# Performance work log

Measured on AMD Instinct MI355X. Metric: run time of the kernel, lower is better.

The kernel has to match this reference:

```python
import jax, jax.numpy as jnp
import numpy as np

L = 32768          # sequence length (keys/values)
E = 1024           # embed_dim (hardcoded in module via weight slices)
H, D = 8, 128      # num_heads, head_dim (hardcoded via reshape(-1, 8, 128))


def setup_inputs() -> dict:
    key = jax.random.key(0)
    k1, k2, k3, k4, k5 = jax.random.split(key, 5)
    scale = 1.0 / np.sqrt(E)
    return {
        "x": jax.random.normal(k1, (L, E), dtype=jnp.float32),
        "in_proj_weight": jax.random.normal(k2, (3 * E, E), dtype=jnp.float32) * scale,
        "in_proj_bias": jax.random.normal(k3, (3 * E,), dtype=jnp.float32) * 0.02,
        "out_proj_weight": jax.random.normal(k4, (E, E), dtype=jnp.float32) * scale,
        "out_proj_bias": jax.random.normal(k5, (E,), dtype=jnp.float32) * 0.02,
    }


def reference(x, in_proj_weight, in_proj_bias, out_proj_weight, out_proj_bias):
    # Single-query (decode-style) attention: q from first token only.
    q = x[:1] @ in_proj_weight[:E].T + in_proj_bias[:E]              # [1, E]
    k = x @ in_proj_weight[E:2 * E].T + in_proj_bias[E:2 * E]        # [L, E]
    v = x @ in_proj_weight[2 * E:].T + in_proj_bias[2 * E:]          # [L, E]

    q = q.reshape(-1, H, D).transpose(1, 0, 2)                       # [H, 1, D]
    k = k.reshape(-1, H, D).transpose(1, 2, 0)                       # [H, D, L]
    v = v.reshape(-1, H, D).transpose(1, 0, 2)                       # [H, L, D]

    dot = jnp.matmul(q, k) * (1.0 / np.sqrt(D))                      # [H, 1, L]
    attn = jax.nn.softmax(dot, axis=-1)
    out = jnp.matmul(attn, v)                                        # [H, 1, D]

    out = out.transpose(1, 0, 2).reshape(-1, E)                      # [1, E]
    out = out @ out_proj_weight.T + out_proj_bias                    # [1, E]
    return out
```

## Files before the change

kernel.cpp:

```cpp
#include <hip/hip_runtime.h>
#include <math.h>


#define L_SEQ   32768
#define E_DIM   1024
#define NHEAD   8
#define HDIM    128
#define TILE_R  8
#define WAVES_M 8

__global__ __launch_bounds__(256) void proj_q(
    const float* __restrict__ W, const float* __restrict__ bias,
    const float* __restrict__ x, float* __restrict__ q)
{
  const int t = threadIdx.x, wave = t >> 6, lane = t & 63;
  const int o = blockIdx.x * 4 + wave;
  const float4* Wr = (const float4*)(W + (size_t)o * E_DIM);
  const float4* xr = (const float4*)x;
  float a = 0.f;
#pragma unroll
  for (int k = 0; k < 4; ++k) {
    float4 wv = Wr[lane + 64 * k];
    float4 xv = xr[lane + 64 * k];
    a += wv.x * xv.x + wv.y * xv.y + wv.z * xv.z + wv.w * xv.w;
  }
#pragma unroll
  for (int m = 1; m < 64; m <<= 1) a += __shfl_xor(a, m, 64);
  if (lane == 0) q[o] = a + bias[o];
}

__global__ __launch_bounds__(128) void make_p(
    const float* __restrict__ W, const float* __restrict__ q,
    float* __restrict__ P_T)
{
  const int h = blockIdx.y;
  const int e = blockIdx.x * 128 + threadIdx.x;
  const float* qh = q + h * HDIM;
  const float* Wb = W + ((size_t)E_DIM + (size_t)h * HDIM) * E_DIM + e;
  float a0 = 0.f, a1 = 0.f, a2 = 0.f, a3 = 0.f;
#pragma unroll 4
  for (int d = 0; d < HDIM; d += 4) {
    a0 += qh[d + 0] * Wb[(size_t)(d + 0) * E_DIM];
    a1 += qh[d + 1] * Wb[(size_t)(d + 1) * E_DIM];
    a2 += qh[d + 2] * Wb[(size_t)(d + 2) * E_DIM];
    a3 += qh[d + 3] * Wb[(size_t)(d + 3) * E_DIM];
  }
  P_T[h * E_DIM + e] = ((a0 + a1) + (a2 + a3)) * 0.08838834764831845f;
}

__global__ __launch_bounds__(512, 2) void attn_fused5(
    const float* __restrict__ x,
    const float* __restrict__ P_T,
    float* __restrict__ partial_z,
    float* __restrict__ partial_sumw,
    int rows_per_blk)
{
  __shared__ __align__(16) float x_tile[2][TILE_R][E_DIM];
  __shared__ __align__(16) float w_tile[TILE_R][NHEAD];
  __shared__ __align__(16) float sw_stage[WAVES_M][4];

  const int t = threadIdx.x;
  const int wave = t >> 6;
  const int lane = t & 63;
  const size_t row0 = (size_t)blockIdx.x * rows_per_blk;
  const int ntiles = rows_per_blk / TILE_R;
  const int rg = wave >> 1;
  const int hg = wave & 1;

  const int r_l = lane & 1;
  const int h_l = (((lane >> 1) & 1) << 1) | ((lane >> 2) & 1);

  float4 p[4][4];
#pragma unroll
  for (int j = 0; j < 4; ++j) {
    const float4* pr = (const float4*)(P_T + (size_t)(4 * hg + j) * E_DIM);
#pragma unroll
    for (int k = 0; k < 4; ++k) p[j][k] = pr[lane + 64 * k];
  }

  float acc[16];
#pragma unroll
  for (int i = 0; i < 16; ++i) acc[i] = 0.f;
  float sumw_own = 0.f;

  {
    const float* g = x + (row0 + wave) * E_DIM;
#pragma unroll
    for (int k = 0; k < 4; ++k)
      __builtin_amdgcn_global_load_lds(
          (const __attribute__((address_space(1))) void*)(g + k * 256 + lane * 4),
          (__attribute__((address_space(3))) void*)(&x_tile[0][wave][k * 256]),
          16, 0, 0);
  }

  for (int tile = 0; tile < ntiles; ++tile) {
    const int buf = tile & 1;
    __syncthreads();

    if (tile + 1 < ntiles) {
      const float* g = x + (row0 + (size_t)(tile + 1) * TILE_R + wave) * E_DIM;
#pragma unroll
      for (int k = 0; k < 4; ++k)
        __builtin_amdgcn_global_load_lds(
            (const __attribute__((address_space(1))) void*)(g + k * 256 + lane * 4),
            (__attribute__((address_space(3))) void*)(&x_tile[buf ^ 1][wave][k * 256]),
            16, 0, 0);
    }

    float v[8];
#pragma unroll
    for (int i = 0; i < 8; ++i) v[i] = 0.f;
#pragma unroll
    for (int r = 0; r < 2; ++r) {
      const float4* xr = (const float4*)&x_tile[buf][2 * rg + r][0];
#pragma unroll
      for (int k = 0; k < 4; ++k) {
        const float4 xv = xr[lane + 64 * k];
#pragma unroll
        for (int j = 0; j < 4; ++j)
          v[r * 4 + j] += xv.x * p[j][k].x + xv.y * p[j][k].y +
                          xv.z * p[j][k].z + xv.w * p[j][k].w;
      }
    }
#pragma unroll
    for (int lev = 0; lev < 3; ++lev) {
      const int d = 1 << lev;
      const int half = 4 >> lev;
#pragma unroll
      for (int i = 0; i < half; ++i) {
        float lo = v[i], hi = v[i + half];
        float keep = (lane & d) ? hi : lo;
        float oth  = (lane & d) ? lo : hi;
        v[i] = keep + __shfl_xor(oth, d, 64);
      }
    }
    float tot = v[0];
    tot += __shfl_xor(tot, 8, 64);
    tot += __shfl_xor(tot, 16, 64);
    tot += __shfl_xor(tot, 32, 64);

    const float w = __expf(tot);
    sumw_own += w;
    if (lane < 8) w_tile[2 * rg + r_l][4 * hg + h_l] = w;

    __syncthreads();

    const float wv = ((const float*)w_tile)[lane];
#pragma unroll
    for (int r = 0; r < TILE_R; ++r) {
      const float2 x2 = *(const float2*)&x_tile[buf][r][2 * t];
#pragma unroll
      for (int h = 0; h < NHEAD; ++h) {
        const float wr = __int_as_float(
            __builtin_amdgcn_readlane(__float_as_int(wv), r * NHEAD + h));
        acc[2 * h]     += wr * x2.x;
        acc[2 * h + 1] += wr * x2.y;
      }
    }
  }

  {
    float* zd = partial_z + (size_t)blockIdx.x * (NHEAD * E_DIM) + 2 * t;
#pragma unroll
    for (int h = 0; h < NHEAD; ++h)
      *(float2*)(zd + h * E_DIM) = make_float2(acc[2 * h], acc[2 * h + 1]);
  }

  {
    float s2 = sumw_own + __shfl_xor(sumw_own, 1, 64);
    if (lane < 8 && (lane & 1) == 0) sw_stage[wave][h_l] = s2;
  }
  __syncthreads();
  if (t < NHEAD) {
    const int hgq = t >> 2, hlq = t & 3;
    float s = 0.f;
#pragma unroll
    for (int rgq = 0; rgq < 4; ++rgq) s += sw_stage[rgq * 2 + hgq][hlq];
    partial_sumw[blockIdx.x * NHEAD + t] = s;
  }
}

__global__ __launch_bounds__(256) void reduce_z(
    const float* __restrict__ partial_z,
    const float* __restrict__ partial_sumw,
    float* __restrict__ zn, int nblk)
{
  __shared__ float red[256];
  __shared__ __align__(16) float swst[4][NHEAD];
  __shared__ float sumw_s[NHEAD];
  const int t = threadIdx.x;
  const int lane = t & 63, wave = t >> 6;

  float sw[NHEAD];
#pragma unroll
  for (int h = 0; h < NHEAD; ++h) sw[h] = 0.f;
  for (int b = t; b < nblk; b += 256) {
    const float4* p = (const float4*)(partial_sumw + (size_t)b * NHEAD);
    float4 a0 = p[0], a1 = p[1];
    sw[0] += a0.x; sw[1] += a0.y; sw[2] += a0.z; sw[3] += a0.w;
    sw[4] += a1.x; sw[5] += a1.y; sw[6] += a1.z; sw[7] += a1.w;
  }
#pragma unroll
  for (int m = 1; m < 64; m <<= 1) {
#pragma unroll
    for (int h = 0; h < NHEAD; ++h) sw[h] += __shfl_xor(sw[h], m, 64);
  }
  if (lane == 0) {
#pragma unroll
    for (int h = 0; h < NHEAD; ++h) swst[wave][h] = sw[h];
  }
  __syncthreads();
  if (t < NHEAD) sumw_s[t] = swst[0][t] + swst[1][t] + swst[2][t] + swst[3][t];

  const int o = blockIdx.x * 32 + (t & 31);
  const int g = t >> 5;
  float a = 0.f;
  for (int b = g; b < nblk; b += 8) a += partial_z[(size_t)b * (NHEAD * E_DIM) + o];
  red[t] = a;
  __syncthreads();
  if (t < 32) {
    float s2 = 0.f;
#pragma unroll
    for (int gg = 0; gg < 8; ++gg) s2 += red[gg * 32 + t];
    const int oo = blockIdx.x * 32 + t;
    zn[oo] = s2 / sumw_s[oo >> 10];
  }
}

__global__ __launch_bounds__(256) void proj_v(
    const float* __restrict__ W, const float* __restrict__ bias,
    const float* __restrict__ zn, float* __restrict__ attn)
{
  const int t = threadIdx.x, wave = t >> 6, lane = t & 63;
  const int o = blockIdx.x * 4 + wave;
  const float4* Wr = (const float4*)(W + ((size_t)2 * E_DIM + o) * E_DIM);
  const float4* zr = (const float4*)(zn + (size_t)(o >> 7) * E_DIM);
  float a = 0.f;
#pragma unroll
  for (int k = 0; k < 4; ++k) {
    float4 wv = Wr[lane + 64 * k];
    float4 zv = zr[lane + 64 * k];
    a += wv.x * zv.x + wv.y * zv.y + wv.z * zv.z + wv.w * zv.w;
  }
#pragma unroll
  for (int m = 1; m < 64; m <<= 1) a += __shfl_xor(a, m, 64);
  if (lane == 0) attn[o] = a + bias[2 * E_DIM + o];
}

__global__ __launch_bounds__(256) void proj_o(
    const float* __restrict__ Wo, const float* __restrict__ bo,
    const float* __restrict__ attn, float* __restrict__ out)
{
  const int t = threadIdx.x, wave = t >> 6, lane = t & 63;
  const int o = blockIdx.x * 4 + wave;
  const float4* Wr = (const float4*)(Wo + (size_t)o * E_DIM);
  const float4* vr = (const float4*)attn;
  float a = 0.f;
#pragma unroll
  for (int k = 0; k < 4; ++k) {
    float4 wv = Wr[lane + 64 * k];
    float4 vv = vr[lane + 64 * k];
    a += wv.x * vv.x + wv.y * vv.y + wv.z * vv.z + wv.w * vv.w;
  }
#pragma unroll
  for (int m = 1; m < 64; m <<= 1) a += __shfl_xor(a, m, 64);
  if (lane == 0) out[o] = a + bo[o];
}

extern "C" void kernel_launch(void* const* d_in, const int* in_sizes, int n_in,
                              void* d_out, int out_size, void* d_ws, size_t ws_size,
                              hipStream_t stream)
{
  const float* x  = (const float*)d_in[0];
  const float* Wi = (const float*)d_in[1];
  const float* bi = (const float*)d_in[2];
  const float* Wo = (const float*)d_in[3];
  const float* bo = (const float*)d_in[4];
  float* out = (float*)d_out;

  char* ws = (char*)d_ws;
  float* q     = (float*)(ws + 0);
  float* P_T   = (float*)(ws + 4096);
  float* zn    = (float*)(ws + 36864);
  float* attn  = (float*)(ws + 69632);
  float* psumw = (float*)(ws + 73728);
  const size_t pz_off = 90112;
  float* pz    = (float*)(ws + pz_off);

  int nblk = 128;
  if (ws_size >= pz_off + (size_t)512 * NHEAD * E_DIM * 4) nblk = 512;
  else if (ws_size >= pz_off + (size_t)256 * NHEAD * E_DIM * 4) nblk = 256;
  const int rows_per_blk = L_SEQ / nblk;

  proj_q     <<<256, 256, 0, stream>>>(Wi, bi, x, q);
  make_p     <<<dim3(8, 8), 128, 0, stream>>>(Wi, q, P_T);
  attn_fused5<<<nblk, 512, 0, stream>>>(x, P_T, pz, psumw, rows_per_blk);
  reduce_z   <<<256, 256, 0, stream>>>(pz, psumw, zn, nblk);
  proj_v     <<<256, 256, 0, stream>>>(Wi, bi, zn, attn);
  proj_o     <<<256, 256, 0, stream>>>(Wo, bo, attn, out);
}
```

Before: 247.3 us.

## Restructure fused attention kernel to 256 threads, 4-row tiles, more blocks

Rewrites the main attention kernel to use 256-thread blocks, with each wave handling two heads over all four rows of a smaller 4-row tile. Each thread now accumulates a float4 slice per head instead of a float2. The block count rises to up to 1024 to fill the machine, which also enlarges the partial-z workspace and the reduction work. The make_p kernel is also unrolled to 8 accumulators. The aim is more parallelism and fewer per-block registers for P, at the cost of more partial sums to reduce and more frequent barriers.

```diff
diff --git a/kernel.cpp b/kernel.cpp
--- a/kernel.cpp
+++ b/kernel.cpp
@@ -6,8 +6,7 @@
 #define E_DIM   1024
 #define NHEAD   8
 #define HDIM    128
-#define TILE_R  8
-#define WAVES_M 8
+#define TILE_R  4
 
 __global__ __launch_bounds__(256) void proj_q(
     const float* __restrict__ W, const float* __restrict__ bias,
@@ -37,18 +36,20 @@
   const int e = blockIdx.x * 128 + threadIdx.x;
   const float* qh = q + h * HDIM;
   const float* Wb = W + ((size_t)E_DIM + (size_t)h * HDIM) * E_DIM + e;
-  float a0 = 0.f, a1 = 0.f, a2 = 0.f, a3 = 0.f;
-#pragma unroll 4
-  for (int d = 0; d < HDIM; d += 4) {
-    a0 += qh[d + 0] * Wb[(size_t)(d + 0) * E_DIM];
-    a1 += qh[d + 1] * Wb[(size_t)(d + 1) * E_DIM];
-    a2 += qh[d + 2] * Wb[(size_t)(d + 2) * E_DIM];
-    a3 += qh[d + 3] * Wb[(size_t)(d + 3) * E_DIM];
-  }
-  P_T[h * E_DIM + e] = ((a0 + a1) + (a2 + a3)) * 0.08838834764831845f;
-}
-
-__global__ __launch_bounds__(512, 2) void attn_fused5(
+  float a[8];
+#pragma unroll
+  for (int j = 0; j < 8; ++j) a[j] = 0.f;
+#pragma unroll 2
+  for (int d = 0; d < HDIM; d += 8) {
+#pragma unroll
+    for (int j = 0; j < 8; ++j)
+      a[j] += qh[d + j] * Wb[(size_t)(d + j) * E_DIM];
+  }
+  const float s = ((a[0] + a[1]) + (a[2] + a[3])) + ((a[4] + a[5]) + (a[6] + a[7]));
+  P_T[h * E_DIM + e] = s * 0.08838834764831845f;
+}
+
+__global__ __launch_bounds__(256, 2) void attn_f6(
     const float* __restrict__ x,
     const float* __restrict__ P_T,
     float* __restrict__ partial_z,
@@ -56,40 +57,38 @@
     int rows_per_blk)
 {
   __shared__ __align__(16) float x_tile[2][TILE_R][E_DIM];
-  __shared__ __align__(16) float w_tile[TILE_R][NHEAD];
-  __shared__ __align__(16) float sw_stage[WAVES_M][4];
+  __shared__ __align__(16) float w_tile[2][TILE_R][NHEAD];
+  __shared__ __align__(16) float sw_stage[4][2];
 
   const int t = threadIdx.x;
-  const int wave = t >> 6;
+  const int j = t >> 6;
   const int lane = t & 63;
   const size_t row0 = (size_t)blockIdx.x * rows_per_blk;
   const int ntiles = rows_per_blk / TILE_R;
-  const int rg = wave >> 1;
-  const int hg = wave & 1;
-
-  const int r_l = lane & 1;
-  const int h_l = (((lane >> 1) & 1) << 1) | ((lane >> 2) & 1);
-
-  float4 p[4][4];
-#pragma unroll
-  for (int j = 0; j < 4; ++j) {
-    const float4* pr = (const float4*)(P_T + (size_t)(4 * hg + j) * E_DIM);
-#pragma unroll
-    for (int k = 0; k < 4; ++k) p[j][k] = pr[lane + 64 * k];
-  }
-
-  float acc[16];
-#pragma unroll
-  for (int i = 0; i < 16; ++i) acc[i] = 0.f;
+
+  const int r_l  = ((lane & 1) << 1) | ((lane >> 1) & 1);
+  const int hp_l = (lane >> 2) & 1;
+
+  float4 p0[4], p1[4];
+  {
+    const float4* pr0 = (const float4*)(P_T + (size_t)(2 * j) * E_DIM) + lane;
+    const float4* pr1 = (const float4*)(P_T + (size_t)(2 * j + 1) * E_DIM) + lane;
+#pragma unroll
+    for (int k = 0; k < 4; ++k) { p0[k] = pr0[64 * k]; p1[k] = pr1[64 * k]; }
+  }
+
+  float4 acc[NHEAD];
+#pragma unroll
+  for (int h = 0; h < NHEAD; ++h) acc[h] = make_float4(0.f, 0.f, 0.f, 0.f);
   float sumw_own = 0.f;
 
   {
-    const float* g = x + (row0 + wave) * E_DIM;
+    const float* g = x + (row0 + j) * E_DIM;
 #pragma unroll
     for (int k = 0; k < 4; ++k)
       __builtin_amdgcn_global_load_lds(
           (const __attribute__((address_space(1))) void*)(g + k * 256 + lane * 4),
-          (__attribute__((address_space(3))) void*)(&x_tile[0][wave][k * 256]),
+          (__attribute__((address_space(3))) void*)(&x_tile[0][j][k * 256]),
           16, 0, 0);
   }
 
@@ -98,30 +97,30 @@
     __syncthreads();
 
     if (tile + 1 < ntiles) {
-      const float* g = x + (row0 + (size_t)(tile + 1) * TILE_R + wave) * E_DIM;
+      const float* g = x + (row0 + (size_t)(tile + 1) * TILE_R + j) * E_DIM;
 #pragma unroll
       for (int k = 0; k < 4; ++k)
         __builtin_amdgcn_global_load_lds(
             (const __attribute__((address_space(1))) void*)(g + k * 256 + lane * 4),
-            (__attribute__((address_space(3))) void*)(&x_tile[buf ^ 1][wave][k * 256]),
+            (__attribute__((address_space(3))) void*)(&x_tile[buf ^ 1][j][k * 256]),
             16, 0, 0);
     }
 
     float v[8];
 #pragma unroll
-    for (int i = 0; i < 8; ++i) v[i] = 0.f;
-#pragma unroll
-    for (int r = 0; r < 2; ++r) {
-      const float4* xr = (const float4*)&x_tile[buf][2 * rg + r][0];
+    for (int r = 0; r < TILE_R; ++r) {
+      const float4* xr = (const float4*)&x_tile[buf][r][0];
+      float a0 = 0.f, a1 = 0.f;
 #pragma unroll
       for (int k = 0; k < 4; ++k) {
         const float4 xv = xr[lane + 64 * k];
-#pragma unroll
-        for (int j = 0; j < 4; ++j)
-          v[r * 4 + j] += xv.x * p[j][k].x + xv.y * p[j][k].y +
-                          xv.z * p[j][k].z + xv.w * p[j][k].w;
+        a0 += xv.x * p0[k].x + xv.y * p0[k].y + xv.z * p0[k].z + xv.w * p0[k].w;
+        a1 += xv.x * p1[k].x + xv.y * p1[k].y + xv.z * p1[k].z + xv.w * p1[k].w;
       }
+      v[r * 2 + 0] = a0;
+      v[r * 2 + 1] = a1;
     }
+
 #pragma unroll
     for (int lev = 0; lev < 3; ++lev) {
       const int d = 1 << lev;
@@ -141,43 +140,43 @@
 
     const float w = __expf(tot);
     sumw_own += w;
-    if (lane < 8) w_tile[2 * rg + r_l][4 * hg + h_l] = w;
+    if (lane < 8) w_tile[buf][r_l][2 * j + hp_l] = w;
 
     __syncthreads();
 
-    const float wv = ((const float*)w_tile)[lane];
+    const float wv32 = ((const float*)w_tile[buf])[lane & 31];
+    const int wi = __float_as_int(wv32);
 #pragma unroll
     for (int r = 0; r < TILE_R; ++r) {
-      const float2 x2 = *(const float2*)&x_tile[buf][r][2 * t];
+      const float4 x4 = *(const float4*)&x_tile[buf][r][4 * t];
 #pragma unroll
       for (int h = 0; h < NHEAD; ++h) {
-        const float wr = __int_as_float(
-            __builtin_amdgcn_readlane(__float_as_int(wv), r * NHEAD + h));
-        acc[2 * h]     += wr * x2.x;
-        acc[2 * h + 1] += wr * x2.y;
+        const float wr = __int_as_float(__builtin_amdgcn_readlane(wi, r * NHEAD + h));
+        acc[h].x += wr * x4.x;
+        acc[h].y += wr * x4.y;
+        acc[h].z += wr * x4.z;
+        acc[h].w += wr * x4.w;
       }
     }
   }
 
   {
-    float* zd = partial_z + (size_t)blockIdx.x * (NHEAD * E_DIM) + 2 * t;
+    float* base = partial_z + (size_t)blockIdx.x * (NHEAD * E_DIM);
 #pragma unroll
     for (int h = 0; h < NHEAD; ++h)
-      *(float2*)(zd + h * E_DIM) = make_float2(acc[2 * h], acc[2 * h + 1]);
+      *(float4*)(base + (size_t)h * E_DIM + 4 * t) = acc[h];
   }
 
   {
-    float s2 = sumw_own + __shfl_xor(sumw_own, 1, 64);
-    if (lane < 8 && (lane & 1) == 0) sw_stage[wave][h_l] = s2;
+    float s = sumw_own;
+    s += __shfl_xor(s, 1, 64);
+    s += __shfl_xor(s, 2, 64);
+    if (lane == 0) sw_stage[j][0] = s;
+    if (lane == 4) sw_stage[j][1] = s;
   }
   __syncthreads();
-  if (t < NHEAD) {
-    const int hgq = t >> 2, hlq = t & 3;
-    float s = 0.f;
-#pragma unroll
-    for (int rgq = 0; rgq < 4; ++rgq) s += sw_stage[rgq * 2 + hgq][hlq];
-    partial_sumw[blockIdx.x * NHEAD + t] = s;
-  }
+  if (t < NHEAD)
+    partial_sumw[(size_t)blockIdx.x * NHEAD + t] = sw_stage[t >> 1][t & 1];
 }
 
 __global__ __launch_bounds__(256) void reduce_z(
@@ -284,18 +283,18 @@
   float* zn    = (float*)(ws + 36864);
   float* attn  = (float*)(ws + 69632);
   float* psumw = (float*)(ws + 73728);
-  const size_t pz_off = 90112;
+  const size_t pz_off = 131072;
   float* pz    = (float*)(ws + pz_off);
 
-  int nblk = 128;
-  if (ws_size >= pz_off + (size_t)512 * NHEAD * E_DIM * 4) nblk = 512;
-  else if (ws_size >= pz_off + (size_t)256 * NHEAD * E_DIM * 4) nblk = 256;
+  int nblk = 256;
+  if (ws_size >= pz_off + (size_t)1024 * NHEAD * E_DIM * 4) nblk = 1024;
+  else if (ws_size >= pz_off + (size_t)512 * NHEAD * E_DIM * 4) nblk = 512;
   const int rows_per_blk = L_SEQ / nblk;
 
-  proj_q     <<<256, 256, 0, stream>>>(Wi, bi, x, q);
-  make_p     <<<dim3(8, 8), 128, 0, stream>>>(Wi, q, P_T);
-  attn_fused5<<<nblk, 512, 0, stream>>>(x, P_T, pz, psumw, rows_per_blk);
-  reduce_z   <<<256, 256, 0, stream>>>(pz, psumw, zn, nblk);
-  proj_v     <<<256, 256, 0, stream>>>(Wi, bi, zn, attn);
-  proj_o     <<<256, 256, 0, stream>>>(Wo, bo, attn, out);
-}
+  proj_q  <<<256, 256, 0, stream>>>(Wi, bi, x, q);
+  make_p  <<<dim3(8, 8), 128, 0, stream>>>(Wi, q, P_T);
+  attn_f6 <<<nblk, 256, 0, stream>>>(x, P_T, pz, psumw, rows_per_blk);
+  reduce_z<<<256, 256, 0, stream>>>(pz, psumw, zn, nblk);
+  proj_v  <<<256, 256, 0, stream>>>(Wi, bi, zn, attn);
+  proj_o  <<<256, 256, 0, stream>>>(Wo, bo, attn, out);
+}
```

After: 258.7 us. +4.6%, slower.
